# Optimization experiments

Measured on AMD Instinct MI355X. Metric: run time of the kernel, lower is better.

The kernel has to match this reference:

```python
import jax, jax.numpy as jnp
import numpy as np

B, S, D = 1, 2048, 1024
H, DH = 16, 64
FF_INNER = 4 * D          # 4096
FUSED = 2 * FF_INNER      # 8192
ROT_BASE = 1000.0


def _rope_tables(seq_len, dim_head):
    # rotarizer: inv_freq = (base ** (arange(0, dh, 2)/dh)) ** -1 ; cached in bfloat16
    inv_freq = 1.0 / (ROT_BASE ** (jnp.arange(0, dim_head, 2, dtype=jnp.float32) / dim_head))
    t = jnp.arange(seq_len, dtype=jnp.float32)
    freqs = jnp.outer(t, inv_freq)                     # [S, DH/2]
    cos = jnp.cos(freqs).astype(jnp.bfloat16)[None, :, None, :]  # [1,S,1,DH/2]
    sin = jnp.sin(freqs).astype(jnp.bfloat16)[None, :, None, :]
    return cos, sin


def _apply_rope(x, cos, sin):
    d = x.shape[-1] // 2
    x1, x2 = x[..., :d], x[..., d:]
    y1 = x1 * cos + x2 * sin
    y2 = -x1 * sin + x2 * cos
    return jnp.concatenate([y1, y2], axis=-1).astype(x.dtype)


def _l2norm(x):
    # F.normalize(p=2, dim=-1), eps=1e-12
    n = jnp.linalg.norm(x, axis=-1, keepdims=True)
    return x / jnp.maximum(n, 1e-12)


def setup_inputs() -> dict:
    key = jax.random.key(0)
    ks = jax.random.split(key, 12)
    std = 0.02
    inp = {
        "h_states": jax.random.normal(ks[0], (B, S, D), jnp.float32),
        "Wq": jax.random.normal(ks[1], (D, D), jnp.float32) * std,
        "Wk": jax.random.normal(ks[2], (D, D), jnp.float32) * std,
        "Wv": jax.random.normal(ks[3], (D, D), jnp.float32) * std,
        "Wqb": jax.random.normal(ks[4], (D, D), jnp.float32) * std,
        "Wkb": jax.random.normal(ks[5], (D, D), jnp.float32) * std,
        "Wo": jax.random.normal(ks[6], (D, D), jnp.float32) * std,
        "bo": jnp.zeros((D,), jnp.float32),
        "W1": jax.random.normal(ks[7], (D, FUSED), jnp.float32) * std,
        "b1": jnp.zeros((FUSED,), jnp.float32),
        "W2": jax.random.normal(ks[8], (FF_INNER, D), jnp.float32) * std,
        "b2": jnp.zeros((D,), jnp.float32),
        "learnedlambda": jnp.asarray(1.0, jnp.float32),
        # l2normscale init: log(S^2 - S) for training_seqlen S
        "l2normscale": jnp.asarray(np.log(float(S) ** 2 - float(S)), np.float32),
    }
    return inp


def reference(h_states, Wq, Wk, Wv, Wqb, Wkb, Wo, bo, W1, b1, W2, b2, learnedlambda, l2normscale):
    b, s, d = h_states.shape
    scale = DH ** -0.5

    # layerwisenorm: RMSNorm, no affine
    eps = jnp.finfo(h_states.dtype).eps
    x = h_states * jax.lax.rsqrt(jnp.mean(jnp.square(h_states), axis=-1, keepdims=True) + eps)

    # projections -> [B,S,H,DH]
    def proj(W):
        return (x @ W).reshape(b, s, H, DH)
    q, k, v = proj(Wq), proj(Wk), proj(Wv)
    qb, kb = proj(Wqb), proj(Wkb)

    cos, sin = _rope_tables(s, DH)
    # per-head qk-norm (l2norm) then rope; v untouched
    q = _apply_rope(_l2norm(q), cos, sin)
    k = _apply_rope(_l2norm(k), cos, sin)
    qb = _apply_rope(_l2norm(qb), cos, sin)
    kb = _apply_rope(_l2norm(kb), cos, sin)

    causal = jnp.tril(jnp.ones((s, s), bool))  # [S,S]

    # main attention: scale=1 (l2norm path), causal softmax, scaled by l2normscale
    scores = jnp.einsum("bqhd,bkhd->bhqk", q, k)
    scores = jnp.where(causal[None, None], scores, -jnp.inf)
    attn = jax.nn.softmax(scores, axis=-1)
    y = l2normscale * jnp.einsum("bhqk,bkhd->bhqd", attn, v)  # [B,H,S,DH]

    # bias attention: masked raw scores @ ones == causal row-sum, broadcast over DH
    sb = jnp.einsum("bqhd,bkhd->bhqk", qb, kb) * scale
    sb = jnp.where(causal[None, None], sb, 0.0)
    y = y + jnp.sum(sb, axis=-1, keepdims=True)  # broadcast over head dim

    y = y.transpose(0, 2, 1, 3).reshape(b, s, d)
    attn_out = y @ Wo + bo

    # fused SwiGLU: chunk -> (x_part, gate); silu(gate) * x_part
    u = x @ W1 + b1
    xp, gate = u[..., :FF_INNER], u[..., FF_INNER:]
    ff = (jax.nn.silu(gate) * xp) @ W2 + b2

    return h_states * learnedlambda + ff + attn_out
```

## Files before the change

### kernel.cpp

```cpp
#include <hip/hip_runtime.h>
#include <hip/hip_bf16.h>
#include <math.h>

typedef __bf16 bf16x8 __attribute__((ext_vector_type(8)));
typedef float  f32x4  __attribute__((ext_vector_type(4)));

#define GLD16(g, l) __builtin_amdgcn_global_load_lds(                      \
    (const __attribute__((address_space(1))) void*)(g),                    \
    (__attribute__((address_space(3))) void*)(l), 16, 0, 0)


__device__ __forceinline__ void tconv_tile(const float* __restrict__ in,
                                           __bf16* __restrict__ out,
                                           int ldin, int ldout,
                                           int r0, int c0, int tid) {
  __shared__ float t[32][33];
  int tx = tid & 31, ty = tid >> 5;
  #pragma unroll
  for (int i = ty; i < 32; i += 8)
    t[i][tx] = in[(size_t)(r0 + i) * ldin + c0 + tx];
  __syncthreads();
  #pragma unroll
  for (int i = ty; i < 32; i += 8)
    out[(size_t)(c0 + i) * ldout + r0 + tx] = (__bf16)t[tx][i];
}

__global__ __launch_bounds__(256) void tconv_k(const float* __restrict__ in,
                                               __bf16* __restrict__ out,
                                               int ldin, int ldout) {
  tconv_tile(in, out, ldin, ldout, blockIdx.y * 32, blockIdx.x * 32, threadIdx.x);
}

__global__ __launch_bounds__(256) void tconv5_k(const float* __restrict__ w0,
    const float* __restrict__ w1, const float* __restrict__ w2,
    const float* __restrict__ w3, const float* __restrict__ w4,
    __bf16* __restrict__ out) {
  const float* src[5] = {w0, w1, w2, w3, w4};
  int z = blockIdx.z;
  tconv_tile(src[z], out + (size_t)z * 1048576, 1024, 1024,
             blockIdx.y * 32, blockIdx.x * 32, threadIdx.x);
}

__global__ __launch_bounds__(256) void tconvwow2_k(const float* __restrict__ Wo,
    const float* __restrict__ W2, __bf16* __restrict__ WoW2t) {
  int tid = threadIdx.x;
  if (blockIdx.z == 0) {
    if (blockIdx.y >= 32) return;
    __shared__ float t[32][33];
    int r0 = blockIdx.y * 32, c0 = blockIdx.x * 32;
    int tx = tid & 31, ty = tid >> 5;
    #pragma unroll
    for (int i = ty; i < 32; i += 8)
      t[i][tx] = Wo[(size_t)(r0 + i) * 1024 + c0 + tx];
    __syncthreads();
    #pragma unroll
    for (int i = ty; i < 32; i += 8)
      WoW2t[(size_t)(c0 + i) * 5120 + r0 + tx] = (__bf16)t[tx][i];
  } else {
    __shared__ float t[32][33];
    int r0 = blockIdx.y * 32, c0 = blockIdx.x * 32;
    int tx = tid & 31, ty = tid >> 5;
    #pragma unroll
    for (int i = ty; i < 32; i += 8)
      t[i][tx] = W2[(size_t)(r0 + i) * 1024 + c0 + tx];
    __syncthreads();
    #pragma unroll
    for (int i = ty; i < 32; i += 8)
      WoW2t[(size_t)(c0 + i) * 5120 + 1024 + r0 + tx] = (__bf16)t[tx][i];
  }
}

__global__ __launch_bounds__(256) void rmsnorm_k(const float* __restrict__ hs,
                                                 __bf16* __restrict__ x) {
  int row = blockIdx.x, tid = threadIdx.x;
  const float4 v = ((const float4*)(hs + (size_t)row * 1024))[tid];
  float ss = v.x * v.x + v.y * v.y + v.z * v.z + v.w * v.w;
  #pragma unroll
  for (int o = 32; o > 0; o >>= 1) ss += __shfl_xor(ss, o);
  __shared__ float ps[4];
  if ((tid & 63) == 0) ps[tid >> 6] = ss;
  __syncthreads();
  float tot = ps[0] + ps[1] + ps[2] + ps[3];
  float r = rsqrtf(tot * (1.0f / 1024.0f) + 1.1920929e-7f);
  __bf16* xr = x + (size_t)row * 1024 + tid * 4;
  xr[0] = (__bf16)(v.x * r); xr[1] = (__bf16)(v.y * r);
  xr[2] = (__bf16)(v.z * r); xr[3] = (__bf16)(v.w * r);
}

__global__ __launch_bounds__(256) void gemm_bt_k(
    const __bf16* __restrict__ A, const __bf16* __restrict__ Bt,
    float* __restrict__ C, int N, int K) {
  __shared__ __bf16 sA[2][128 * 32];
  __shared__ __bf16 sB[2][128 * 32];
  const int tid = threadIdx.x;
  const int lane = tid & 63;
  const int quad = lane >> 4, l16 = lane & 15;
  const int wave = tid >> 6;
  const int waveM = wave >> 1, waveN = wave & 1;
  const int m0 = blockIdx.y * 128, n0 = blockIdx.x * 128;
  const int nk = K >> 5;
  const int rowS = tid >> 2;
  const int kg = ((tid & 3) ^ ((rowS >> 1) & 3)) * 8;
  const __bf16* gA0 = A + (size_t)(m0 + rowS) * K + kg;
  const __bf16* gA1 = gA0 + (size_t)64 * K;
  const __bf16* gB0 = Bt + (size_t)(n0 + rowS) * K + kg;
  const __bf16* gB1 = gB0 + (size_t)64 * K;
  const int lo0 = tid * 8, lo1 = 2048 + tid * 8;

  GLD16(gA0, sA[0] + lo0);
  GLD16(gA1, sA[0] + lo1);
  GLD16(gB0, sB[0] + lo0);
  GLD16(gB1, sB[0] + lo1);

  f32x4 acc[4][4] = {};
  for (int i = 0; i < nk; ++i) {
    __syncthreads();
    if (i + 1 < nk) {
      const int k = (i + 1) * 32;
      __bf16* dA = sA[(i + 1) & 1];
      __bf16* dB = sB[(i + 1) & 1];
      GLD16(gA0 + k, dA + lo0);
      GLD16(gA1 + k, dA + lo1);
      GLD16(gB0 + k, dB + lo0);
      GLD16(gB1 + k, dB + lo1);
    }
    const __bf16* cA = sA[i & 1];
    const __bf16* cB = sB[i & 1];
    bf16x8 af[4], bfv[4];
    #pragma unroll
    for (int mt = 0; mt < 4; ++mt) {
      int r = waveM * 64 + mt * 16 + l16;
      af[mt] = *(const bf16x8*)(cA + r * 32 + ((quad ^ ((r >> 1) & 3)) * 8));
    }
    #pragma unroll
    for (int nt = 0; nt < 4; ++nt) {
      int r = waveN * 64 + nt * 16 + l16;
      bfv[nt] = *(const bf16x8*)(cB + r * 32 + ((quad ^ ((r >> 1) & 3)) * 8));
    }
    #pragma unroll
    for (int mt = 0; mt < 4; ++mt)
      #pragma unroll
      for (int nt = 0; nt < 4; ++nt)
        acc[mt][nt] = __builtin_amdgcn_mfma_f32_16x16x32_bf16(af[mt], bfv[nt], acc[mt][nt], 0, 0, 0);
  }
  #pragma unroll
  for (int mt = 0; mt < 4; ++mt) {
    int row = m0 + waveM * 64 + mt * 16 + quad * 4;
    #pragma unroll
    for (int nt = 0; nt < 4; ++nt) {
      int col = n0 + waveN * 64 + nt * 16 + l16;
      #pragma unroll
      for (int r = 0; r < 4; ++r)
        C[(size_t)(row + r) * N + col] = acc[mt][nt][r];
    }
  }
}

__global__ __launch_bounds__(256) void gemm_partk_k(
    const __bf16* __restrict__ A, const __bf16* __restrict__ Bt,
    float* __restrict__ P, int N, int K) {
  __shared__ __bf16 sA[2][128 * 32];
  __shared__ __bf16 sB[2][128 * 32];
  const int tid = threadIdx.x;
  const int lane = tid & 63;
  const int quad = lane >> 4, l16 = lane & 15;
  const int wave = tid >> 6;
  const int waveM = wave >> 1, waveN = wave & 1;
  const int m0 = blockIdx.y * 128, n0 = blockIdx.x * 128;
  const int kz = blockIdx.z, nz = gridDim.z;
  const int kper = K / nz, kbeg = kz * kper;
  const int nk = kper >> 5;
  const size_t MN = (size_t)gridDim.y * 128 * N;
  float* C = P + (size_t)kz * MN;
  const int rowS = tid >> 2;
  const int kg = ((tid & 3) ^ ((rowS >> 1) & 3)) * 8;
  const __bf16* gA0 = A + (size_t)(m0 + rowS) * K + kbeg + kg;
  const __bf16* gA1 = gA0 + (size_t)64 * K;
  const __bf16* gB0 = Bt + (size_t)(n0 + rowS) * K + kbeg + kg;
  const __bf16* gB1 = gB0 + (size_t)64 * K;
  const int lo0 = tid * 8, lo1 = 2048 + tid * 8;

  GLD16(gA0, sA[0] + lo0);
  GLD16(gA1, sA[0] + lo1);
  GLD16(gB0, sB[0] + lo0);
  GLD16(gB1, sB[0] + lo1);

  f32x4 acc[4][4] = {};
  for (int i = 0; i < nk; ++i) {
    __syncthreads();
    if (i + 1 < nk) {
      const int k = (i + 1) * 32;
      __bf16* dA = sA[(i + 1) & 1];
      __bf16* dB = sB[(i + 1) & 1];
      GLD16(gA0 + k, dA + lo0);
      GLD16(gA1 + k, dA + lo1);
      GLD16(gB0 + k, dB + lo0);
      GLD16(gB1 + k, dB + lo1);
    }
    const __bf16* cA = sA[i & 1];
    const __bf16* cB = sB[i & 1];
    bf16x8 af[4], bfv[4];
    #pragma unroll
    for (int mt = 0; mt < 4; ++mt) {
      int r = waveM * 64 + mt * 16 + l16;
      af[mt] = *(const bf16x8*)(cA + r * 32 + ((quad ^ ((r >> 1) & 3)) * 8));
    }
    #pragma unroll
    for (int nt = 0; nt < 4; ++nt) {
      int r = waveN * 64 + nt * 16 + l16;
      bfv[nt] = *(const bf16x8*)(cB + r * 32 + ((quad ^ ((r >> 1) & 3)) * 8));
    }
    #pragma unroll
    for (int mt = 0; mt < 4; ++mt)
      #pragma unroll
      for (int nt = 0; nt < 4; ++nt)
        acc[mt][nt] = __builtin_amdgcn_mfma_f32_16x16x32_bf16(af[mt], bfv[nt], acc[mt][nt], 0, 0, 0);
  }
  #pragma unroll
  for (int mt = 0; mt < 4; ++mt) {
    int row = m0 + waveM * 64 + mt * 16 + quad * 4;
    #pragma unroll
    for (int nt = 0; nt < 4; ++nt) {
      int col = n0 + waveN * 64 + nt * 16 + l16;
      #pragma unroll
      for (int r = 0; r < 4; ++r)
        C[(size_t)(row + r) * N + col] = acc[mt][nt][r];
    }
  }
}

__global__ __launch_bounds__(256) void ffn1silu_k(
    const __bf16* __restrict__ A, const __bf16* __restrict__ W1t,
    const float* __restrict__ b1, __bf16* __restrict__ ffout) {
  __shared__ __bf16 sA[2][128 * 32];
  __shared__ __bf16 sBx[2][64 * 32];
  __shared__ __bf16 sBg[2][64 * 32];
  const int tid = threadIdx.x, lane = tid & 63, w = tid >> 6;
  const int quad = lane >> 4, l16 = lane & 15;
  const int waveM = w >> 1, waveN = w & 1;
  const int m0 = blockIdx.y * 128, n0 = blockIdx.x * 64;
  const int K = 1024, nk = 32;
  const int rowS = tid >> 2;
  const int kg = ((tid & 3) ^ ((rowS >> 1) & 3)) * 8;
  const __bf16* gA0 = A + (size_t)(m0 + rowS) * K + kg;
  const __bf16* gA1 = gA0 + (size_t)64 * K;
  const __bf16* gBx = W1t + (size_t)(n0 + rowS) * K + kg;
  const __bf16* gBg = W1t + (size_t)(4096 + n0 + rowS) * K + kg;
  const int lo0 = tid * 8, lo1 = 2048 + tid * 8;

  GLD16(gA0, sA[0] + lo0);
  GLD16(gA1, sA[0] + lo1);
  GLD16(gBx, sBx[0] + lo0);
  GLD16(gBg, sBg[0] + lo0);

  f32x4 ax[4][2] = {}, ag[4][2] = {};
  for (int i = 0; i < nk; ++i) {
    __syncthreads();
    if (i + 1 < nk) {
      const int k = (i + 1) * 32, b = (i + 1) & 1;
      GLD16(gA0 + k, sA[b] + lo0);
      GLD16(gA1 + k, sA[b] + lo1);
      GLD16(gBx + k, sBx[b] + lo0);
      GLD16(gBg + k, sBg[b] + lo0);
    }
    const __bf16* cA = sA[i & 1];
    const __bf16* cx = sBx[i & 1];
    const __bf16* cg = sBg[i & 1];
    bf16x8 af[4], bx[2], bg[2];
    #pragma unroll
    for (int mt = 0; mt < 4; ++mt) {
      int r = waveM * 64 + mt * 16 + l16;
      af[mt] = *(const bf16x8*)(cA + r * 32 + ((quad ^ ((r >> 1) & 3)) * 8));
    }
    #pragma unroll
    for (int nt = 0; nt < 2; ++nt) {
      int r = waveN * 32 + nt * 16 + l16;
      int sl = (quad ^ ((r >> 1) & 3)) * 8;
      bx[nt] = *(const bf16x8*)(cx + r * 32 + sl);
      bg[nt] = *(const bf16x8*)(cg + r * 32 + sl);
    }
    #pragma unroll
    for (int mt = 0; mt < 4; ++mt)
      #pragma unroll
      for (int nt = 0; nt < 2; ++nt) {
        ax[mt][nt] = __builtin_amdgcn_mfma_f32_16x16x32_bf16(af[mt], bx[nt], ax[mt][nt], 0, 0, 0);
        ag[mt][nt] = __builtin_amdgcn_mfma_f32_16x16x32_bf16(af[mt], bg[nt], ag[mt][nt], 0, 0, 0);
      }
  }
  #pragma unroll
  for (int mt = 0; mt < 4; ++mt) {
    int row = m0 + waveM * 64 + mt * 16 + quad * 4;
    #pragma unroll
    for (int nt = 0; nt < 2; ++nt) {
      int col = n0 + waveN * 32 + nt * 16 + l16;
      float bxv = b1[col], bgv = b1[col + 4096];
      #pragma unroll
      for (int r = 0; r < 4; ++r) {
        float xp = ax[mt][nt][r] + bxv;
        float g  = ag[mt][nt][r] + bgv;
        float val = xp * g / (1.f + __expf(-g));
        ffout[(size_t)(row + r) * 5120 + 1024 + col] = (__bf16)val;
      }
    }
  }
}

__global__ __launch_bounds__(256) void combine_k(
    const float* __restrict__ P, const float* __restrict__ b2,
    const float* __restrict__ bo, const float* __restrict__ hs,
    const float* __restrict__ plam, float* __restrict__ out) {
  const size_t MN = (size_t)2048 * 1024;
  size_t i = ((size_t)blockIdx.x * 256 + threadIdx.x) * 4;
  int col = (int)(i & 1023);
  float4 a0 = *(const float4*)(P + i);
  float4 a1 = *(const float4*)(P + MN + i);
  float4 a2 = *(const float4*)(P + 2 * MN + i);
  float4 a3 = *(const float4*)(P + 3 * MN + i);
  float4 h  = *(const float4*)(hs + i);
  float4 v2 = *(const float4*)(b2 + col);
  float4 vo = *(const float4*)(bo + col);
  float lam = plam[0];
  float4 o;
  o.x = (a0.x + a1.x) + (a2.x + a3.x) + v2.x + vo.x + lam * h.x;
  o.y = (a0.y + a1.y) + (a2.y + a3.y) + v2.y + vo.y + lam * h.y;
  o.z = (a0.z + a1.z) + (a2.z + a3.z) + v2.z + vo.z + lam * h.z;
  o.w = (a0.w + a1.w) + (a2.w + a3.w) + v2.w + vo.w + lam * h.w;
  *(float4*)(out + i) = o;
}

__global__ __launch_bounds__(256) void qkprep_k(const float* __restrict__ proj,
    __bf16* __restrict__ qo, __bf16* __restrict__ ko,
    float* __restrict__ qbo, float* __restrict__ kbo) {
  int gw = blockIdx.x * 4 + (threadIdx.x >> 6);
  int lane = threadIdx.x & 63;
  int s = gw >> 4, h = gw & 15;
  int j = lane & 31;
  float inv = powf(1000.0f, -(float)j * (1.0f / 32.0f));
  float ang = (float)s * inv;
  float cb = (float)(__bf16)cosf(ang);
  float sb = (float)(__bf16)sinf(ang);
  size_t ibase = (size_t)s * 5120 + h * 64 + lane;
  size_t obase = (size_t)s * 1024 + h * 64 + lane;
  bool lo = lane < 32;

  auto proc = [&](const float* src) -> float {
    float xv = src[ibase];
    float ss = xv * xv;
    #pragma unroll
    for (int o = 32; o > 0; o >>= 1) ss += __shfl_xor(ss, o);
    float y = xv / fmaxf(sqrtf(ss), 1e-12f);
    float yp = __shfl_xor(y, 32);
    return lo ? (y * cb + yp * sb) : (y * cb - yp * sb);
  };
  qo[obase]  = (__bf16)proc(proj + 0);
  ko[obase]  = (__bf16)proc(proj + 1024);
  qbo[obase] = proc(proj + 3072);
  kbo[obase] = proc(proj + 4096);
}

__global__ __launch_bounds__(64) void kbsum_k(const float* __restrict__ kb,
                                              float* __restrict__ tsum) {
  int t = blockIdx.x, h = blockIdx.y, d = threadIdx.x;
  size_t base = (size_t)h * 64 + d;
  float s = 0.f;
  #pragma unroll 4
  for (int r = 0; r < 32; ++r)
    s += kb[(size_t)(t * 32 + r) * 1024 + base];
  tsum[(t * 16 + h) * 64 + d] = s;
}

__global__ __launch_bounds__(64) void sbrow2_k(const float* __restrict__ qb,
                                               const float* __restrict__ kb,
                                               const float* __restrict__ tsum,
                                               float* __restrict__ sb) {
  int t = blockIdx.x, h = blockIdx.y, d = threadIdx.x;
  size_t base = (size_t)h * 64 + d;
  float run = 0.f;
  for (int tp = 0; tp < t; ++tp) run += tsum[(tp * 16 + h) * 64 + d];
  for (int s0 = 0; s0 < 32; s0 += 4) {
    float p[4];
    #pragma unroll
    for (int u = 0; u < 4; ++u) {
      size_t off = (size_t)(t * 32 + s0 + u) * 1024 + base;
      run += kb[off];
      p[u] = qb[off] * run;
    }
    #pragma unroll
    for (int o = 32; o > 0; o >>= 1) {
      #pragma unroll
      for (int u = 0; u < 4; ++u) p[u] += __shfl_xor(p[u], o);
    }
    if (d == 0) {
      #pragma unroll
      for (int u = 0; u < 4; ++u) sb[(t * 32 + s0 + u) * 16 + h] = 0.125f * p[u];
    }
  }
}

__global__ __launch_bounds__(256) void attn_k(const __bf16* __restrict__ qg,
    const __bf16* __restrict__ kg, const __bf16* __restrict__ vtg,
    float* __restrict__ o_part, float* __restrict__ m_part,
    float* __restrict__ l_part) {
  __shared__ __bf16 sK[64 * 64];
  __shared__ __bf16 sVt[64 * 64];
  __shared__ __bf16 sP[4][16 * 64];
  const int pair = blockIdx.x, j4 = blockIdx.y, hh = blockIdx.z;
  const int tid = threadIdx.x, lane = tid & 63, w = tid >> 6;
  const int quad = lane >> 4, l16 = lane & 15;
  const int srow = tid >> 3;
  const int sg = (tid & 7) ^ (srow & 7);
  __bf16* ldsK = sK + tid * 8;
  __bf16* ldsV = sVt + tid * 8;
  __bf16* sPw = sP[w];

  for (int phase = 0; phase < 2; ++phase) {
    const int qt = phase ? 31 - pair : pair;
    const int q0 = qt * 64;
    const int n = qt + 1;
    const int kb = (j4 * n) >> 2, ke = ((j4 + 1) * n) >> 2;
    bf16x8 qf[2];
    #pragma unroll
    for (int kk = 0; kk < 2; ++kk)
      qf[kk] = *(const bf16x8*)(qg + (size_t)(q0 + w * 16 + l16) * 1024 + hh * 64 + kk * 32 + quad * 8);
    f32x4 accO[4] = {};
    float m_[4], l_[4];
    #pragma unroll
    for (int r = 0; r < 4; ++r) { m_[r] = -INFINITY; l_[r] = 0.f; }

    for (int kt = kb; kt < ke; ++kt) {
      const __bf16* gK = kg + (size_t)(kt * 64 + srow) * 1024 + hh * 64 + sg * 8;
      const __bf16* gV = vtg + (size_t)(hh * 64 + srow) * 2048 + kt * 64 + sg * 8;
      GLD16(gK, ldsK);
      GLD16(gK + (size_t)32 * 1024, ldsK + 2048);
      GLD16(gV, ldsV);
      GLD16(gV + (size_t)32 * 2048, ldsV + 2048);
      __syncthreads();

      f32x4 s4[4];
      #pragma unroll
      for (int nt = 0; nt < 4; ++nt) {
        int r = nt * 16 + l16;
        bf16x8 b0 = *(const bf16x8*)(sK + r * 64 + ((quad ^ (r & 7)) * 8));
        bf16x8 b1 = *(const bf16x8*)(sK + r * 64 + (((4 + quad) ^ (r & 7)) * 8));
        f32x4 sa = {0.f, 0.f, 0.f, 0.f};
        sa = __builtin_amdgcn_mfma_f32_16x16x32_bf16(qf[0], b0, sa, 0, 0, 0);
        sa = __builtin_amdgcn_mfma_f32_16x16x32_bf16(qf[1], b1, sa, 0, 0, 0);
        s4[nt] = sa;
      }
      if (kt == qt) {
        #pragma unroll
        for (int nt = 0; nt < 4; ++nt)
          #pragma unroll
          for (int r = 0; r < 4; ++r)
            if (nt * 16 + l16 > w * 16 + quad * 4 + r) s4[nt][r] = -INFINITY;
      }
      float mx[4], al[4], rs[4];
      #pragma unroll
      for (int r = 0; r < 4; ++r)
        mx[r] = fmaxf(fmaxf(s4[0][r], s4[1][r]), fmaxf(s4[2][r], s4[3][r]));
      #pragma unroll
      for (int o = 1; o < 16; o <<= 1)
        #pragma unroll
        for (int r = 0; r < 4; ++r) mx[r] = fmaxf(mx[r], __shfl_xor(mx[r], o));
      #pragma unroll
      for (int r = 0; r < 4; ++r) {
        float mn = fmaxf(m_[r], mx[r]);
        al[r] = __expf(m_[r] - mn);
        m_[r] = mn;
      }
      float p[4][4];
      #pragma unroll
      for (int nt = 0; nt < 4; ++nt)
        #pragma unroll
        for (int r = 0; r < 4; ++r)
          p[nt][r] = __expf(s4[nt][r] - m_[r]);
      #pragma unroll
      for (int r = 0; r < 4; ++r)
        rs[r] = (p[0][r] + p[1][r]) + (p[2][r] + p[3][r]);
      #pragma unroll
      for (int o = 1; o < 16; o <<= 1)
        #pragma unroll
        for (int r = 0; r < 4; ++r) rs[r] += __shfl_xor(rs[r], o);
      #pragma unroll
      for (int r = 0; r < 4; ++r) l_[r] = l_[r] * al[r] + rs[r];
      #pragma unroll
      for (int nt = 0; nt < 4; ++nt)
        #pragma unroll
        for (int r = 0; r < 4; ++r) accO[nt][r] *= al[r];
      #pragma unroll
      for (int nt = 0; nt < 4; ++nt)
        #pragma unroll
        for (int r = 0; r < 4; ++r) {
          int row = quad * 4 + r, col = nt * 16 + l16;
          sPw[row * 64 + (col ^ ((row & 7) << 3))] = (__bf16)p[nt][r];
        }
      #pragma unroll
      for (int kk = 0; kk < 2; ++kk) {
        bf16x8 a = *(const bf16x8*)(sPw + l16 * 64 + (((kk * 4 + quad) ^ (l16 & 7)) * 8));
        #pragma unroll
        for (int nt = 0; nt < 4; ++nt) {
          int vr = nt * 16 + l16;
          bf16x8 bv = *(const bf16x8*)(sVt + vr * 64 + (((kk * 4 + quad) ^ (vr & 7)) * 8));
          accO[nt] = __builtin_amdgcn_mfma_f32_16x16x32_bf16(a, bv, accO[nt], 0, 0, 0);
        }
      }
      __syncthreads();
    }
    #pragma unroll
    for (int r = 0; r < 4; ++r) {
      int grow = q0 + w * 16 + quad * 4 + r;
      if (l16 == 0) {
        m_part[((size_t)j4 * 2048 + grow) * 16 + hh] = m_[r];
        l_part[((size_t)j4 * 2048 + grow) * 16 + hh] = l_[r];
      }
      #pragma unroll
      for (int nt = 0; nt < 4; ++nt)
        o_part[((size_t)j4 * 2048 + grow) * 1024 + hh * 64 + nt * 16 + l16] = accO[nt][r];
    }
  }
}

__global__ __launch_bounds__(256) void attnmerge_k(const float* __restrict__ o_part,
    const float* __restrict__ m_part, const float* __restrict__ l_part,
    const float* __restrict__ sbr, const float* __restrict__ pl2s,
    __bf16* __restrict__ yo) {
  int idx = blockIdx.x * 256 + threadIdx.x;
  int s = idx >> 8, rem = idx & 255;
  int h = rem >> 4, dg = (rem & 15) * 4;
  float m[4], l[4];
  #pragma unroll
  for (int j = 0; j < 4; ++j) {
    m[j] = m_part[((size_t)j * 2048 + s) * 16 + h];
    l[j] = l_part[((size_t)j * 2048 + s) * 16 + h];
  }
  float M = fmaxf(fmaxf(m[0], m[1]), fmaxf(m[2], m[3]));
  float den = 0.f;
  float4 acc = {0.f, 0.f, 0.f, 0.f};
  #pragma unroll
  for (int j = 0; j < 4; ++j) {
    float e = __expf(m[j] - M);
    den += l[j] * e;
    float4 o = *(const float4*)(o_part + ((size_t)j * 2048 + s) * 1024 + h * 64 + dg);
    acc.x += e * o.x; acc.y += e * o.y; acc.z += e * o.z; acc.w += e * o.w;
  }
  float sc = pl2s[0] / den;
  float add = sbr[s * 16 + h];
  __bf16* yp = yo + (size_t)s * 5120 + h * 64 + dg;
  yp[0] = (__bf16)(sc * acc.x + add);
  yp[1] = (__bf16)(sc * acc.y + add);
  yp[2] = (__bf16)(sc * acc.z + add);
  yp[3] = (__bf16)(sc * acc.w + add);
}

extern "C" void kernel_launch(void* const* d_in, const int* in_sizes, int n_in,
                              void* d_out, int out_size, void* d_ws, size_t ws_size,
                              hipStream_t stream) {
  (void)in_sizes; (void)n_in; (void)out_size; (void)ws_size;
  const float* hs   = (const float*)d_in[0];
  const float* Wq   = (const float*)d_in[1];
  const float* Wk   = (const float*)d_in[2];
  const float* Wv   = (const float*)d_in[3];
  const float* Wqb  = (const float*)d_in[4];
  const float* Wkb  = (const float*)d_in[5];
  const float* Wo   = (const float*)d_in[6];
  const float* bo   = (const float*)d_in[7];
  const float* W1   = (const float*)d_in[8];
  const float* b1   = (const float*)d_in[9];
  const float* W2   = (const float*)d_in[10];
  const float* b2   = (const float*)d_in[11];
  const float* plam = (const float*)d_in[12];
  const float* pl2s = (const float*)d_in[13];
  float* out = (float*)d_out;
  char* ws = (char*)d_ws;

  size_t off = 0;
  auto alloc = [&](size_t bytes) { char* p = ws + off; off += (bytes + 255) & ~(size_t)255; return p; };
  __bf16* Wt5    = (__bf16*)alloc((size_t)5 * 1024 * 1024 * 2);
  __bf16* WoW2t  = (__bf16*)alloc((size_t)1024 * 5120 * 2);
  __bf16* W1t    = (__bf16*)alloc((size_t)8192 * 1024 * 2);
  __bf16* xbf    = (__bf16*)alloc((size_t)2048 * 1024 * 2);
  __bf16* concat = (__bf16*)alloc((size_t)2048 * 5120 * 2);
  float*  proj  = (float*)alloc((size_t)2048 * 5120 * 4);
  float*  qbf32 = (float*)alloc((size_t)2048 * 1024 * 4);
  float*  kbf32 = (float*)alloc((size_t)2048 * 1024 * 4);
  __bf16* qbf   = (__bf16*)alloc((size_t)2048 * 1024 * 2);
  __bf16* kbf   = (__bf16*)alloc((size_t)2048 * 1024 * 2);
  float*  o_part = proj;
  float*  m_part = qbf32;
  float*  l_part = qbf32 + (size_t)4 * 2048 * 16;
  float*  gpart  = proj;
  __bf16* vtbf  = (__bf16*)alloc((size_t)1024 * 2048 * 2);
  float*  sbrow = (float*)alloc((size_t)2048 * 16 * 4);
  float*  tsum  = (float*)alloc((size_t)64 * 16 * 64 * 4);

  tconv5_k<<<dim3(32, 32, 5), 256, 0, stream>>>(Wq, Wk, Wv, Wqb, Wkb, Wt5);
  tconvwow2_k<<<dim3(32, 128, 2), 256, 0, stream>>>(Wo, W2, WoW2t);
  tconv_k<<<dim3(256, 32), 256, 0, stream>>>(W1, W1t, 8192, 1024);

  rmsnorm_k<<<2048, 256, 0, stream>>>(hs, xbf);
  gemm_bt_k<<<dim3(40, 16), 256, 0, stream>>>(xbf, Wt5, proj, 5120, 1024);
  qkprep_k<<<8192, 256, 0, stream>>>(proj, qbf, kbf, qbf32, kbf32);
  tconv_k<<<dim3(32, 64), 256, 0, stream>>>(proj + 2048, vtbf, 5120, 2048);
  kbsum_k<<<dim3(64, 16), 64, 0, stream>>>(kbf32, tsum);
  sbrow2_k<<<dim3(64, 16), 64, 0, stream>>>(qbf32, kbf32, tsum, sbrow);
  attn_k<<<dim3(16, 4, 16), 256, 0, stream>>>(qbf, kbf, vtbf, o_part, m_part, l_part);
  attnmerge_k<<<2048, 256, 0, stream>>>(o_part, m_part, l_part, sbrow, pl2s, concat);
  ffn1silu_k<<<dim3(64, 16), 256, 0, stream>>>(xbf, W1t, b1, concat);
  gemm_partk_k<<<dim3(8, 16, 4), 256, 0, stream>>>(concat, WoW2t, gpart, 1024, 5120);
  combine_k<<<2048, 256, 0, stream>>>(gpart, b2, bo, hs, plam, out);
}
```

Before: 384.5 us.

## Retile FFN1 SwiGLU GEMM to 256x256 blocks with interleaved W1 layout and 4-stage pipeline

The W1 transpose now interleaves x-part and gate columns in 32-column groups, so one contiguous B tile holds both halves. The FFN1+SiLU kernel moves from 128x64 tiles with 256 threads to 256x256 tiles with 512 threads. It uses a 4-deep async LDS ring with explicit vmcnt waits, raw barriers and setprio around the MFMA bursts. This is meant to raise data reuse per loaded byte and hide global-load latency, at the cost of much more LDS (128KB) and registers per block, and only 256 blocks.

Result: faster. 368.2 us (-4.2%).

```diff
diff --git a/kernel.cpp b/kernel.cpp
--- a/kernel.cpp
+++ b/kernel.cpp
@@ -29,6 +29,22 @@
                                                __bf16* __restrict__ out,
                                                int ldin, int ldout) {
   tconv_tile(in, out, ldin, ldout, blockIdx.y * 32, blockIdx.x * 32, threadIdx.x);
+}
+
+__global__ __launch_bounds__(256) void tconvw1p_k(const float* __restrict__ W1,
+                                                  __bf16* __restrict__ out) {
+  int c0 = blockIdx.x * 32;
+  int src_c0 = ((c0 >> 5) & 1) * 4096 + (c0 >> 6) * 32;
+  __shared__ float t[32][33];
+  int r0 = blockIdx.y * 32;
+  int tid = threadIdx.x, tx = tid & 31, ty = tid >> 5;
+  #pragma unroll
+  for (int i = ty; i < 32; i += 8)
+    t[i][tx] = W1[(size_t)(r0 + i) * 8192 + src_c0 + tx];
+  __syncthreads();
+  #pragma unroll
+  for (int i = ty; i < 32; i += 8)
+    out[(size_t)(c0 + i) * 1024 + r0 + tx] = (__bf16)t[tx][i];
 }
 
 __global__ __launch_bounds__(256) void tconv5_k(const float* __restrict__ w0,
@@ -229,75 +245,96 @@
   }
 }
 
-__global__ __launch_bounds__(256) void ffn1silu_k(
+__global__ __launch_bounds__(512, 2) void ffn1silu_k(
     const __bf16* __restrict__ A, const __bf16* __restrict__ W1t,
     const float* __restrict__ b1, __bf16* __restrict__ ffout) {
-  __shared__ __bf16 sA[2][128 * 32];
-  __shared__ __bf16 sBx[2][64 * 32];
-  __shared__ __bf16 sBg[2][64 * 32];
+  __shared__ __bf16 sA[4][256 * 32];
+  __shared__ __bf16 sB[4][256 * 32];
   const int tid = threadIdx.x, lane = tid & 63, w = tid >> 6;
   const int quad = lane >> 4, l16 = lane & 15;
-  const int waveM = w >> 1, waveN = w & 1;
-  const int m0 = blockIdx.y * 128, n0 = blockIdx.x * 64;
-  const int K = 1024, nk = 32;
+  const int wm = w >> 2, wn = w & 3;
+  const int m0 = blockIdx.y * 256;
+  const int n0p = blockIdx.x * 256;
+  const int K = 1024, NKT = 32;
   const int rowS = tid >> 2;
   const int kg = ((tid & 3) ^ ((rowS >> 1) & 3)) * 8;
   const __bf16* gA0 = A + (size_t)(m0 + rowS) * K + kg;
-  const __bf16* gA1 = gA0 + (size_t)64 * K;
-  const __bf16* gBx = W1t + (size_t)(n0 + rowS) * K + kg;
-  const __bf16* gBg = W1t + (size_t)(4096 + n0 + rowS) * K + kg;
-  const int lo0 = tid * 8, lo1 = 2048 + tid * 8;
-
-  GLD16(gA0, sA[0] + lo0);
-  GLD16(gA1, sA[0] + lo1);
-  GLD16(gBx, sBx[0] + lo0);
-  GLD16(gBg, sBg[0] + lo0);
-
-  f32x4 ax[4][2] = {}, ag[4][2] = {};
-  for (int i = 0; i < nk; ++i) {
-    __syncthreads();
-    if (i + 1 < nk) {
-      const int k = (i + 1) * 32, b = (i + 1) & 1;
-      GLD16(gA0 + k, sA[b] + lo0);
-      GLD16(gA1 + k, sA[b] + lo1);
-      GLD16(gBx + k, sBx[b] + lo0);
-      GLD16(gBg + k, sBg[b] + lo0);
-    }
-    const __bf16* cA = sA[i & 1];
-    const __bf16* cx = sBx[i & 1];
-    const __bf16* cg = sBg[i & 1];
-    bf16x8 af[4], bx[2], bg[2];
+  const __bf16* gA1 = gA0 + (size_t)128 * K;
+  const __bf16* gB0 = W1t + (size_t)(n0p + rowS) * K + kg;
+  const __bf16* gB1 = gB0 + (size_t)128 * K;
+  const int lo0 = tid * 8, lo1 = 4096 + tid * 8;
+
+  f32x4 acc[8][4] = {};
+
+  auto stageA = [&](int t) {
+    __bf16* d = sA[t & 3];
+    GLD16(gA0 + t * 32, d + lo0);
+    GLD16(gA1 + t * 32, d + lo1);
+  };
+  auto stageB = [&](int t) {
+    __bf16* d = sB[t & 3];
+    GLD16(gB0 + t * 32, d + lo0);
+    GLD16(gB1 + t * 32, d + lo1);
+  };
+
+  auto compute_half = [&](const __bf16* cA, const __bf16* cB,
+                          const bf16x8* bfr, int half) {
+    bf16x8 af[4];
     #pragma unroll
     for (int mt = 0; mt < 4; ++mt) {
-      int r = waveM * 64 + mt * 16 + l16;
+      int r = wm * 128 + half * 64 + mt * 16 + l16;
       af[mt] = *(const bf16x8*)(cA + r * 32 + ((quad ^ ((r >> 1) & 3)) * 8));
     }
-    #pragma unroll
-    for (int nt = 0; nt < 2; ++nt) {
-      int r = waveN * 32 + nt * 16 + l16;
-      int sl = (quad ^ ((r >> 1) & 3)) * 8;
-      bx[nt] = *(const bf16x8*)(cx + r * 32 + sl);
-      bg[nt] = *(const bf16x8*)(cg + r * 32 + sl);
-    }
+    __builtin_amdgcn_s_setprio(1);
     #pragma unroll
     for (int mt = 0; mt < 4; ++mt)
       #pragma unroll
-      for (int nt = 0; nt < 2; ++nt) {
-        ax[mt][nt] = __builtin_amdgcn_mfma_f32_16x16x32_bf16(af[mt], bx[nt], ax[mt][nt], 0, 0, 0);
-        ag[mt][nt] = __builtin_amdgcn_mfma_f32_16x16x32_bf16(af[mt], bg[nt], ag[mt][nt], 0, 0, 0);
-      }
-  }
-  #pragma unroll
-  for (int mt = 0; mt < 4; ++mt) {
-    int row = m0 + waveM * 64 + mt * 16 + quad * 4;
-    #pragma unroll
-    for (int nt = 0; nt < 2; ++nt) {
-      int col = n0 + waveN * 32 + nt * 16 + l16;
+      for (int nt = 0; nt < 4; ++nt)
+        acc[half * 4 + mt][nt] = __builtin_amdgcn_mfma_f32_16x16x32_bf16(
+            af[mt], bfr[nt], acc[half * 4 + mt][nt], 0, 0, 0);
+    __builtin_amdgcn_s_setprio(0);
+  };
+
+  stageA(0); stageB(0);
+  stageA(1); stageB(1);
+  stageA(2); stageB(2);
+
+  #pragma unroll 1
+  for (int t = 0; t < NKT; ++t) {
+    if (t < NKT - 2)
+      asm volatile("s_waitcnt vmcnt(8)" ::: "memory");
+    else if (t == NKT - 2)
+      asm volatile("s_waitcnt vmcnt(4)" ::: "memory");
+    else
+      asm volatile("s_waitcnt vmcnt(0)" ::: "memory");
+    __builtin_amdgcn_s_barrier();
+    __builtin_amdgcn_sched_barrier(0);
+    const __bf16* cA = sA[t & 3];
+    const __bf16* cB = sB[t & 3];
+    if (t + 3 < NKT) stageA(t + 3);
+    bf16x8 bfr[4];
+    #pragma unroll
+    for (int nt = 0; nt < 4; ++nt) {
+      int r = wn * 64 + nt * 16 + l16;
+      bfr[nt] = *(const bf16x8*)(cB + r * 32 + ((quad ^ ((r >> 1) & 3)) * 8));
+    }
+    compute_half(cA, cB, bfr, 0);
+    if (t + 3 < NKT) stageB(t + 3);
+    compute_half(cA, cB, bfr, 1);
+  }
+
+  const int colbase = (blockIdx.x * 4 + wn) * 32;
+  #pragma unroll
+  for (int j = 0; j < 8; ++j) {
+    int row = m0 + wm * 128 + (j >> 2) * 64 + (j & 3) * 16 + quad * 4;
+    #pragma unroll
+    for (int p = 0; p < 2; ++p) {
+      int col = colbase + p * 16 + l16;
       float bxv = b1[col], bgv = b1[col + 4096];
       #pragma unroll
       for (int r = 0; r < 4; ++r) {
-        float xp = ax[mt][nt][r] + bxv;
-        float g  = ag[mt][nt][r] + bgv;
+        float xp = acc[j][p][r] + bxv;
+        float g  = acc[j][p + 2][r] + bgv;
         float val = xp * g / (1.f + __expf(-g));
         ffout[(size_t)(row + r) * 5120 + 1024 + col] = (__bf16)val;
       }
@@ -595,7 +632,7 @@
 
   tconv5_k<<<dim3(32, 32, 5), 256, 0, stream>>>(Wq, Wk, Wv, Wqb, Wkb, Wt5);
   tconvwow2_k<<<dim3(32, 128, 2), 256, 0, stream>>>(Wo, W2, WoW2t);
-  tconv_k<<<dim3(256, 32), 256, 0, stream>>>(W1, W1t, 8192, 1024);
+  tconvw1p_k<<<dim3(256, 32), 256, 0, stream>>>(W1, W1t);
 
   rmsnorm_k<<<2048, 256, 0, stream>>>(hs, xbf);
   gemm_bt_k<<<dim3(40, 16), 256, 0, stream>>>(xbf, Wt5, proj, 5120, 1024);
@@ -605,7 +642,7 @@
   sbrow2_k<<<dim3(64, 16), 64, 0, stream>>>(qbf32, kbf32, tsum, sbrow);
   attn_k<<<dim3(16, 4, 16), 256, 0, stream>>>(qbf, kbf, vtbf, o_part, m_part, l_part);
   attnmerge_k<<<2048, 256, 0, stream>>>(o_part, m_part, l_part, sbrow, pl2s, concat);
-  ffn1silu_k<<<dim3(64, 16), 256, 0, stream>>>(xbf, W1t, b1, concat);
+  ffn1silu_k<<<dim3(32, 8), 512, 0, stream>>>(xbf, W1t, b1, concat);
   gemm_partk_k<<<dim3(8, 16, 4), 256, 0, stream>>>(concat, WoW2t, gpart, 1024, 5120);
   combine_k<<<2048, 256, 0, stream>>>(gpart, b2, bo, hs, plam, out);
 }
```
